# Performance work log

Hardware: AMD Instinct MI355X
Metric: run time of the kernel (lower is better)

Reference implementation:

```python
import jax, jax.numpy as jnp
import numpy as np

ALPHA = 0.2          # LeakyReLU slope
THRESH = 0.6         # adjacency connection threshold
NEG_INF = -9e15      # masked-softmax fill used by the original


def setup_inputs() -> dict:
    key = jax.random.key(0)
    ks = jax.random.split(key, 5)
    B, N, F = 32, 512, 128
    h = jax.random.normal(ks[0], (B, N, F), dtype=jnp.float32)
    # torch nn.Linear weights: y = x @ W.T
    W = jax.random.normal(ks[1], (F, F), dtype=jnp.float32) * 0.1
    a = jax.random.normal(ks[2], (2 * F, 1), dtype=jnp.float32) * 0.1
    A0 = jax.random.normal(ks[3], (4 * N, N), dtype=jnp.float32) * 0.05
    A2 = jax.random.normal(ks[4], (N, 4 * N), dtype=jnp.float32) * 0.05
    return {"h": h, "W": W, "a": a, "A0": A0, "A2": A2}


def reference(h, W, a, A0, A2):
    F = W.shape[0]
    # Wh = W(h)                                  [B, N, F]
    Wh = jnp.einsum("bnf,gf->bng", h, W)
    # attention logits e = leakyrelu(Wh a1 + (Wh a2)^T)   [B, N, N]
    Wh1 = Wh @ a[:F]                              # [B, N, 1]
    Wh2 = Wh @ a[F:]                              # [B, N, 1]
    e = jax.nn.leaky_relu(Wh1 + jnp.swapaxes(Wh2, 1, 2), ALPHA)
    # learned adjacency MLP over last (node) dim: Linear -> Sigmoid -> Linear
    adj = e + jnp.einsum("bnk,mk->bnm", jax.nn.sigmoid(jnp.einsum("bnm,km->bnk", e, A0)), A2)
    # threshold + mask + softmax
    adj = jnp.where(adj > THRESH, adj, 0.0)
    att = jnp.where(adj > 0, e, NEG_INF)
    att = jax.nn.softmax(att, axis=2)
    # dropout is identity in eval mode
    h_prime = jnp.einsum("bnm,bmf->bnf", att, Wh)
    return jax.nn.elu(h_prime)                    # concat=True branch
```

## Files before the change

kernel.cpp:

```cpp
#include <hip/hip_runtime.h>

#define BB 32
#define NN 512
#define FF 128
#define K4 2048
#define ALPHA 0.2f
#define THRESH 0.6f
#define NEGINF -9e15f

typedef unsigned short u16;
typedef unsigned int u32;
typedef _Float16 f16;
typedef __attribute__((ext_vector_type(8))) _Float16 half8;
typedef __attribute__((ext_vector_type(4))) float f32x4;

union U16F { u16 u; f16 h; };
__device__ __forceinline__ u16 hbits(f16 h) { U16F x; x.h = h; return x.u; }
__device__ __forceinline__ float htof(u16 u) { U16F x; x.u = u; return (float)x.h; }
__device__ __forceinline__ void split2(float v, u16& hi, u16& lo) {
    f16 h = (f16)v;
    f16 l = (f16)(v - (float)h);
    hi = hbits(h);
    lo = hbits(l);
}
__device__ __forceinline__ float lrelu(float x) { return x > 0.f ? x : ALPHA * x; }

__device__ __forceinline__ void gload16(const void* g, void* l) {
    __builtin_amdgcn_global_load_lds(
        (__attribute__((address_space(1))) const unsigned int*)(unsigned long long)g,
        (__attribute__((address_space(3))) unsigned int*)(unsigned int)(unsigned long long)l,
        16, 0, 0);
}

__global__ void k_u(const float* __restrict__ W, const float* __restrict__ a,
                    float* __restrict__ u12) {
    int f = threadIdx.x;
    float s1 = 0.f, s2 = 0.f;
    for (int g = 0; g < FF; ++g) {
        float w = W[g * FF + f];
        s1 += w * a[g];
        s2 += w * a[FF + g];
    }
    u12[f] = s1;
    u12[FF + f] = s2;
}

__global__ void k_wh12(const float* __restrict__ h, const float* __restrict__ u12,
                       float* __restrict__ Wh12) {
    int row = blockIdx.x;
    int f = threadIdx.x;
    float hv = h[(size_t)row * FF + f];
    float p1 = hv * u12[f], p2 = hv * u12[FF + f];
#pragma unroll
    for (int o = 1; o < 64; o <<= 1) {
        p1 += __shfl_xor(p1, o, 64);
        p2 += __shfl_xor(p2, o, 64);
    }
    __shared__ float s1[2], s2[2];
    int w = f >> 6;
    if ((f & 63) == 0) { s1[w] = p1; s2[w] = p2; }
    __syncthreads();
    if (f == 0) {
        Wh12[row] = s1[0] + s1[1];
        Wh12[BB * NN + row] = s2[0] + s2[1];
    }
}

__global__ __launch_bounds__(256) void k_whT(const float* __restrict__ W,
                                             const float* __restrict__ h,
                                             u16* __restrict__ Thi, u16* __restrict__ Tlo) {
    const int bm = blockIdx.y * 64, bn = blockIdx.x * 64;
    __shared__ float As[32][68];
    __shared__ float Bs[32][68];
    int tid = threadIdx.x;
    int tx = tid & 15, ty = tid >> 4;
    float acc[4][4] = {{0.f}};
    int r = tid >> 3, q = tid & 7;
    const float* Ap = W + (size_t)(bm + r) * FF + q * 4;
    const float* Bp = h + (size_t)(bn + r) * FF + q * 4;
    for (int k0 = 0; k0 < FF; k0 += 32) {
        float4 a0 = *(const float4*)(Ap + k0);
        float4 a1 = *(const float4*)(Ap + k0 + 32 * FF);
        float4 b0 = *(const float4*)(Bp + k0);
        float4 b1 = *(const float4*)(Bp + k0 + 32 * FF);
        __syncthreads();
        As[q * 4 + 0][r] = a0.x; As[q * 4 + 1][r] = a0.y;
        As[q * 4 + 2][r] = a0.z; As[q * 4 + 3][r] = a0.w;
        As[q * 4 + 0][r + 32] = a1.x; As[q * 4 + 1][r + 32] = a1.y;
        As[q * 4 + 2][r + 32] = a1.z; As[q * 4 + 3][r + 32] = a1.w;
        Bs[q * 4 + 0][r] = b0.x; Bs[q * 4 + 1][r] = b0.y;
        Bs[q * 4 + 2][r] = b0.z; Bs[q * 4 + 3][r] = b0.w;
        Bs[q * 4 + 0][r + 32] = b1.x; Bs[q * 4 + 1][r + 32] = b1.y;
        Bs[q * 4 + 2][r + 32] = b1.z; Bs[q * 4 + 3][r + 32] = b1.w;
        __syncthreads();
#pragma unroll
        for (int kk = 0; kk < 32; ++kk) {
            float av[4], bv[4];
            *(float4*)av = *(const float4*)&As[kk][ty * 4];
            *(float4*)bv = *(const float4*)&Bs[kk][tx * 4];
#pragma unroll
            for (int i = 0; i < 4; ++i)
#pragma unroll
                for (int j = 0; j < 4; ++j) acc[i][j] = fmaf(av[i], bv[j], acc[i][j]);
        }
    }
#pragma unroll
    for (int i = 0; i < 4; ++i) {
        int f = bm + ty * 4 + i;
#pragma unroll
        for (int j = 0; j < 4; ++j) {
            int mg = bn + tx * 4 + j;
            u16 hi, lo;
            split2(acc[i][j], hi, lo);
            size_t idx = ((size_t)(mg >> 9) * FF + f) * NN + (mg & 511);
            Thi[idx] = hi;
            Tlo[idx] = lo;
        }
    }
}

__global__ void k_split(const float* __restrict__ X, u16* __restrict__ Hi,
                        u16* __restrict__ Lo, int n4) {
    int i = blockIdx.x * 256 + threadIdx.x;
    if (i >= n4) return;
    float4 v = *(const float4*)(X + (size_t)i * 4);
    ushort4 hh, ll;
    split2(v.x, hh.x, ll.x);
    split2(v.y, hh.y, ll.y);
    split2(v.z, hh.z, ll.z);
    split2(v.w, hh.w, ll.w);
    *(ushort4*)(Hi + (size_t)i * 4) = hh;
    *(ushort4*)(Lo + (size_t)i * 4) = ll;
}

__global__ __launch_bounds__(512, 2) void k_g1(const float* __restrict__ Wh12, int c0,
                                               const u16* __restrict__ Bhi,
                                               const u16* __restrict__ Blo,
                                               u16* __restrict__ Shi, u16* __restrict__ Slo,
                                               int mblocks) {
    __shared__ __align__(16) u16 lds[2][4][8192];
    __shared__ float wh1s[256];
    __shared__ float wh2s[512];
    const int tid = threadIdx.x;
    const int l = tid & 63, w = tid >> 6;
    const int nwg = gridDim.x, q = nwg >> 3;
    const int wg = (blockIdx.x & 7) * q + (blockIdx.x >> 3);
    const int nb = wg / mblocks, mb = wg % mblocks;
    const int bm = mb * 256, bn = nb * 256;
    const int bglob = c0 + (bm >> 9);

    if (tid < 256) wh1s[tid] = Wh12[(size_t)c0 * NN + bm + tid];
    wh2s[tid] = Wh12[BB * NN + (size_t)bglob * NN + tid];
    if (tid + 512 < 512) {}
    __syncthreads();

    auto GEN_A = [&](int buf, int k0) {
#pragma unroll
        for (int cc = 0; cc < 2; ++cc) {
            const int c = tid + cc * 512;
            const int row = ((c >> 6) << 4) + (c & 15);
            const int kc = k0 + ((c >> 4) & 3) * 8;
            const float w1 = wh1s[row];
            u32 hh[4], llv[4];
#pragma unroll
            for (int jj = 0; jj < 4; ++jj) {
                float e0 = lrelu(w1 + wh2s[kc + 2 * jj]);
                float e1 = lrelu(w1 + wh2s[kc + 2 * jj + 1]);
                u16 h0, l0, h1, l1;
                split2(e0, h0, l0);
                split2(e1, h1, l1);
                hh[jj] = (u32)h0 | ((u32)h1 << 16);
                llv[jj] = (u32)l0 | ((u32)l1 << 16);
            }
            *(uint4*)&lds[buf][0][c * 8] = make_uint4(hh[0], hh[1], hh[2], hh[3]);
            *(uint4*)&lds[buf][1][c * 8] = make_uint4(llv[0], llv[1], llv[2], llv[3]);
        }
    };
    auto STAGE_B = [&](int buf, int k0) {
#pragma unroll
        for (int i = 0; i < 2; ++i) {
            const int g = w * 2 + i;
            const size_t ro = (size_t)(bn + g * 16 + (l & 15)) * NN + k0 + ((l >> 4) * 8);
            gload16(Bhi + ro, &lds[buf][2][g * 512]);
            gload16(Blo + ro, &lds[buf][3][g * 512]);
        }
    };

    f32x4 acc[8][4];
#pragma unroll
    for (int m = 0; m < 8; ++m)
#pragma unroll
        for (int n = 0; n < 4; ++n) acc[m][n] = (f32x4){0.f, 0.f, 0.f, 0.f};

    GEN_A(0, 0);
    STAGE_B(0, 0);
    for (int t = 0; t < 16; ++t) {
        const int cur = t & 1;
        if (t < 15) {
            GEN_A(cur ^ 1, (t + 1) * 32);
            STAGE_B(cur ^ 1, (t + 1) * 32);
            asm volatile("s_waitcnt vmcnt(4)" ::: "memory");
        } else {
            asm volatile("s_waitcnt vmcnt(0)" ::: "memory");
        }
        asm volatile("s_waitcnt lgkmcnt(0)" ::: "memory");
        __builtin_amdgcn_s_barrier();
        __builtin_amdgcn_sched_barrier(0);
        half8 bh[4], bl[4];
#pragma unroll
        for (int n = 0; n < 4; ++n) {
            const int gB = (w & 3) * 4 + n;
            bh[n] = *(const half8*)&lds[cur][2][(gB * 64 + l) * 8];
            bl[n] = *(const half8*)&lds[cur][3][(gB * 64 + l) * 8];
        }
        __builtin_amdgcn_s_setprio(1);
#pragma unroll
        for (int m = 0; m < 8; ++m) {
            const int gA = (w >> 2) * 8 + m;
            half8 ah = *(const half8*)&lds[cur][0][(gA * 64 + l) * 8];
            half8 al = *(const half8*)&lds[cur][1][(gA * 64 + l) * 8];
#pragma unroll
            for (int n = 0; n < 4; ++n) {
                acc[m][n] =
                    __builtin_amdgcn_mfma_f32_16x16x32_f16(ah, bh[n], acc[m][n], 0, 0, 0);
                acc[m][n] =
                    __builtin_amdgcn_mfma_f32_16x16x32_f16(al, bh[n], acc[m][n], 0, 0, 0);
                acc[m][n] =
                    __builtin_amdgcn_mfma_f32_16x16x32_f16(ah, bl[n], acc[m][n], 0, 0, 0);
            }
        }
        __builtin_amdgcn_s_setprio(0);
        __builtin_amdgcn_sched_barrier(0);
        __builtin_amdgcn_s_barrier();
    }

    const int lr = (l >> 4) * 4, lc = l & 15;
#pragma unroll
    for (int m = 0; m < 8; ++m) {
#pragma unroll
        for (int n = 0; n < 4; ++n) {
#pragma unroll
            for (int j = 0; j < 4; ++j) {
                const int row = bm + (w >> 2) * 128 + m * 16 + lr + j;
                const int col = bn + (w & 3) * 64 + n * 16 + lc;
                const float s = 1.f / (1.f + expf(-acc[m][n][j]));
                u16 hi, lo;
                split2(s, hi, lo);
                const size_t idx = (size_t)row * K4 + col;
                Shi[idx] = hi;
                Slo[idx] = lo;
            }
        }
    }
}

__global__ __launch_bounds__(512, 2) void k_g2(const u16* __restrict__ Ahi,
                                               const u16* __restrict__ Alo,
                                               const u16* __restrict__ Bhi,
                                               const u16* __restrict__ Blo,
                                               const float* __restrict__ Wh12, int c0,
                                               u32* __restrict__ ADJ, int mblocks) {
    __shared__ __align__(16) u16 ldsA[2][2][4096];
    __shared__ __align__(16) u16 ldsB[2][2][8192];
    const int tid = threadIdx.x;
    const int l = tid & 63, w = tid >> 6;
    const int nwg = gridDim.x, q = nwg >> 3;
    const int wg = (blockIdx.x & 7) * q + (blockIdx.x >> 3);
    const int nb = wg / mblocks, mb = wg % mblocks;
    const int bm = mb * 128, bn = nb * 256;

    auto STAGE = [&](int buf, int k0) {
        const size_t ra = (size_t)(bm + w * 16 + (l & 15)) * K4 + k0 + ((l >> 4) * 8);
        gload16(Ahi + ra, &ldsA[buf][0][w * 512]);
        gload16(Alo + ra, &ldsA[buf][1][w * 512]);
#pragma unroll
        for (int i = 0; i < 2; ++i) {
            const int g = w * 2 + i;
            const size_t rb = (size_t)(bn + g * 16 + (l & 15)) * K4 + k0 + ((l >> 4) * 8);
            gload16(Bhi + rb, &ldsB[buf][0][g * 512]);
            gload16(Blo + rb, &ldsB[buf][1][g * 512]);
        }
    };

    f32x4 acc[4][4];
#pragma unroll
    for (int m = 0; m < 4; ++m)
#pragma unroll
        for (int n = 0; n < 4; ++n) acc[m][n] = (f32x4){0.f, 0.f, 0.f, 0.f};

    STAGE(0, 0);
    for (int t = 0; t < 64; ++t) {
        const int cur = t & 1;
        if (t < 63) {
            STAGE(cur ^ 1, (t + 1) * 32);
            asm volatile("s_waitcnt vmcnt(6)" ::: "memory");
        } else {
            asm volatile("s_waitcnt vmcnt(0)" ::: "memory");
        }
        __builtin_amdgcn_s_barrier();
        __builtin_amdgcn_sched_barrier(0);
        half8 bh[4], bl[4];
#pragma unroll
        for (int n = 0; n < 4; ++n) {
            const int gB = (w & 3) * 4 + n;
            bh[n] = *(const half8*)&ldsB[cur][0][(gB * 64 + l) * 8];
            bl[n] = *(const half8*)&ldsB[cur][1][(gB * 64 + l) * 8];
        }
        __builtin_amdgcn_s_setprio(1);
#pragma unroll
        for (int m = 0; m < 4; ++m) {
            const int gA = (w >> 2) * 4 + m;
            half8 ah = *(const half8*)&ldsA[cur][0][(gA * 64 + l) * 8];
            half8 al = *(const half8*)&ldsA[cur][1][(gA * 64 + l) * 8];
#pragma unroll
            for (int n = 0; n < 4; ++n) {
                acc[m][n] =
                    __builtin_amdgcn_mfma_f32_16x16x32_f16(ah, bh[n], acc[m][n], 0, 0, 0);
                acc[m][n] =
                    __builtin_amdgcn_mfma_f32_16x16x32_f16(al, bh[n], acc[m][n], 0, 0, 0);
                acc[m][n] =
                    __builtin_amdgcn_mfma_f32_16x16x32_f16(ah, bl[n], acc[m][n], 0, 0, 0);
            }
        }
        __builtin_amdgcn_s_setprio(0);
        __builtin_amdgcn_sched_barrier(0);
        __builtin_amdgcn_s_barrier();
    }

    const int bglob = c0 + (bm >> 9);
    const float* wh2p = Wh12 + BB * NN + (size_t)bglob * NN;
    const int lr = (l >> 4) * 4, lc = l & 15;
#pragma unroll
    for (int m = 0; m < 4; ++m) {
#pragma unroll
        for (int n = 0; n < 4; ++n) {
#pragma unroll
            for (int j = 0; j < 4; ++j) {
                const int row = bm + (w >> 2) * 64 + m * 16 + lr + j;
                const int col = bn + (w & 3) * 64 + n * 16 + lc;
                const float e = lrelu(Wh12[(size_t)c0 * NN + row] + wh2p[col]);
                u32 pk = 0xFFFFFFFFu;
                if (e + acc[m][n][j] > THRESH) {
                    u16 hi, lo;
                    split2(e, hi, lo);
                    pk = (u32)hi | ((u32)lo << 16);
                }
                ADJ[(size_t)row * NN + col] = pk;
            }
        }
    }
}

__global__ __launch_bounds__(256) void k_softmax2(const u32* __restrict__ ADJ,
                                                  u16* __restrict__ Hi, u16* __restrict__ Lo) {
    const size_t row = blockIdx.x;
    const u32* p = ADJ + row * NN;
    const int t = threadIdx.x;
    u32 w0 = p[t], w1 = p[t + 256];
    float v0 = (w0 == 0xFFFFFFFFu) ? NEGINF : htof((u16)(w0 & 0xFFFF)) + htof((u16)(w0 >> 16));
    float v1 = (w1 == 0xFFFFFFFFu) ? NEGINF : htof((u16)(w1 & 0xFFFF)) + htof((u16)(w1 >> 16));
    float m = fmaxf(v0, v1);
#pragma unroll
    for (int o = 1; o < 64; o <<= 1) m = fmaxf(m, __shfl_xor(m, o, 64));
    __shared__ float red[4], red2[4];
    int w = t >> 6;
    if ((t & 63) == 0) red[w] = m;
    __syncthreads();
    m = fmaxf(fmaxf(red[0], red[1]), fmaxf(red[2], red[3]));
    float e0 = __expf(v0 - m), e1 = __expf(v1 - m);
    float s = e0 + e1;
#pragma unroll
    for (int o = 1; o < 64; o <<= 1) s += __shfl_xor(s, o, 64);
    if ((t & 63) == 0) red2[w] = s;
    __syncthreads();
    s = red2[0] + red2[1] + red2[2] + red2[3];
    float inv = 1.f / s;
    float a0 = e0 * inv, a1 = e1 * inv;
    u16 h0, l0, h1, l1;
    split2(a0, h0, l0);
    split2(a1, h1, l1);
    Hi[row * NN + t] = h0;
    Hi[row * NN + t + 256] = h1;
    Lo[row * NN + t] = l0;
    Lo[row * NN + t + 256] = l1;
}

__global__ __launch_bounds__(256) void k_pv(const u16* __restrict__ Ahi,
                                            const u16* __restrict__ Alo,
                                            const u16* __restrict__ Bhi,
                                            const u16* __restrict__ Blo,
                                            float* __restrict__ OUT) {
    __shared__ __align__(16) u16 lds[2][4][4096];
    const int tid = threadIdx.x;
    const int l = tid & 63, w = tid >> 6;
    const int wr = w >> 1, wc = w & 1;
    const int bz = blockIdx.z;
    const int bm = blockIdx.y * 128, bn = 0;

    const u16* A0p = Ahi + (size_t)bz * NN * NN;
    const u16* A1p = Alo + (size_t)bz * NN * NN;
    const u16* B0p = Bhi + (size_t)bz * FF * NN;
    const u16* B1p = Blo + (size_t)bz * FF * NN;

    const int g0 = w, g1 = w + 4;
    const size_t offA0 = (size_t)(bm + g0 * 16 + (l & 15)) * NN + (l >> 4) * 8;
    const size_t offA1 = (size_t)(bm + g1 * 16 + (l & 15)) * NN + (l >> 4) * 8;
    const size_t offB0 = (size_t)(bn + g0 * 16 + (l & 15)) * NN + (l >> 4) * 8;
    const size_t offB1 = (size_t)(bn + g1 * 16 + (l & 15)) * NN + (l >> 4) * 8;

    auto STAGE = [&](int buf, int kk) {
        gload16(A0p + offA0 + kk, &lds[buf][0][g0 * 512]);
        gload16(A0p + offA1 + kk, &lds[buf][0][g1 * 512]);
        gload16(A1p + offA0 + kk, &lds[buf][1][g0 * 512]);
        gload16(A1p + offA1 + kk, &lds[buf][1][g1 * 512]);
        gload16(B0p + offB0 + kk, &lds[buf][2][g0 * 512]);
        gload16(B0p + offB1 + kk, &lds[buf][2][g1 * 512]);
        gload16(B1p + offB0 + kk, &lds[buf][3][g0 * 512]);
        gload16(B1p + offB1 + kk, &lds[buf][3][g1 * 512]);
    };

    f32x4 acc[4][4];
#pragma unroll
    for (int m = 0; m < 4; ++m)
#pragma unroll
        for (int n = 0; n < 4; ++n) acc[m][n] = (f32x4){0.f, 0.f, 0.f, 0.f};

    STAGE(0, 0);
    for (int t = 0; t < 16; ++t) {
        const int cur = t & 1;
        if (t + 1 < 16) {
            STAGE(cur ^ 1, (t + 1) * 32);
            asm volatile("s_waitcnt vmcnt(8)" ::: "memory");
        } else {
            asm volatile("s_waitcnt vmcnt(0)" ::: "memory");
        }
        __builtin_amdgcn_s_barrier();
        __builtin_amdgcn_sched_barrier(0);
        half8 ah[4], al[4], bh[4], bl[4];
#pragma unroll
        for (int m = 0; m < 4; ++m) {
            ah[m] = *(const half8*)&lds[cur][0][((wr * 4 + m) * 64 + l) * 8];
            al[m] = *(const half8*)&lds[cur][1][((wr * 4 + m) * 64 + l) * 8];
        }
#pragma unroll
        for (int n = 0; n < 4; ++n) {
            bh[n] = *(const half8*)&lds[cur][2][((wc * 4 + n) * 64 + l) * 8];
            bl[n] = *(const half8*)&lds[cur][3][((wc * 4 + n) * 64 + l) * 8];
        }
#pragma unroll
        for (int m = 0; m < 4; ++m)
#pragma unroll
            for (int n = 0; n < 4; ++n) {
                acc[m][n] =
                    __builtin_amdgcn_mfma_f32_16x16x32_f16(ah[m], bh[n], acc[m][n], 0, 0, 0);
                acc[m][n] =
                    __builtin_amdgcn_mfma_f32_16x16x32_f16(al[m], bh[n], acc[m][n], 0, 0, 0);
                acc[m][n] =
                    __builtin_amdgcn_mfma_f32_16x16x32_f16(ah[m], bl[n], acc[m][n], 0, 0, 0);
            }
        __builtin_amdgcn_s_barrier();
    }

    const int lr = (l >> 4) * 4, lc = l & 15;
#pragma unroll
    for (int m = 0; m < 4; ++m) {
#pragma unroll
        for (int n = 0; n < 4; ++n) {
#pragma unroll
            for (int j = 0; j < 4; ++j) {
                const int row = bm + wr * 64 + m * 16 + lr + j;
                const int col = bn + wc * 64 + n * 16 + lc;
                const float v = acc[m][n][j];
                OUT[(size_t)bz * NN * FF + (size_t)row * FF + col] =
                    v > 0.f ? v : __expf(v) - 1.f;
            }
        }
    }
}

extern "C" void kernel_launch(void* const* d_in, const int* in_sizes, int n_in,
                              void* d_out, int out_size, void* d_ws, size_t ws_size,
                              hipStream_t stream) {
    const float* h = (const float*)d_in[0];
    const float* W = (const float*)d_in[1];
    const float* a = (const float*)d_in[2];
    const float* A0 = (const float*)d_in[3];
    const float* A2 = (const float*)d_in[4];
    float* out = (float*)d_out;

    char* ws = (char*)d_ws;
    size_t ofs = 0;
    auto alloc = [&](size_t bytes) -> void* {
        void* p = ws + ofs;
        ofs = (ofs + bytes + 255) & ~(size_t)255;
        return p;
    };
    float* u12 = (float*)alloc(2 * FF * sizeof(float));
    float* Wh12 = (float*)alloc(2 * (size_t)BB * NN * sizeof(float));
    u16* WhThi = (u16*)alloc((size_t)BB * FF * NN * 2);
    u16* WhTlo = (u16*)alloc((size_t)BB * FF * NN * 2);
    u16* A0hi = (u16*)alloc((size_t)K4 * NN * 2);
    u16* A0lo = (u16*)alloc((size_t)K4 * NN * 2);
    u16* A2hi = (u16*)alloc((size_t)NN * K4 * 2);
    u16* A2lo = (u16*)alloc((size_t)NN * K4 * 2);

    const size_t per_b =
        (size_t)NN * K4 * 2 * 2 + (size_t)NN * NN * 4 + (size_t)NN * NN * 2 * 2;
    int cb = BB;
    while (cb > 1 && ofs + (size_t)cb * per_b + 8192 > ws_size) cb >>= 1;
    u16* Shi = (u16*)alloc((size_t)cb * NN * K4 * 2);
    u16* Slo = (u16*)alloc((size_t)cb * NN * K4 * 2);
    u32* ADJ = (u32*)alloc((size_t)cb * NN * NN * 4);
    u16* AttHi = (u16*)alloc((size_t)cb * NN * NN * 2);
    u16* AttLo = (u16*)alloc((size_t)cb * NN * NN * 2);

    k_u<<<1, 128, 0, stream>>>(W, a, u12);
    k_wh12<<<BB * NN, 128, 0, stream>>>(h, u12, Wh12);
    k_whT<<<dim3((BB * NN) / 64, FF / 64), 256, 0, stream>>>(W, h, WhThi, WhTlo);
    k_split<<<(K4 * NN / 4 + 255) / 256, 256, 0, stream>>>(A0, A0hi, A0lo, K4 * NN / 4);
    k_split<<<(NN * K4 / 4 + 255) / 256, 256, 0, stream>>>(A2, A2hi, A2lo, NN * K4 / 4);

    for (int c0 = 0; c0 < BB; c0 += cb) {
        const int c = (BB - c0) < cb ? (BB - c0) : cb;
        const int mb1 = c * 2;
        const int mb2 = c * 4;
        k_g1<<<mb1 * (K4 / 256), 512, 0, stream>>>(Wh12, c0, A0hi, A0lo, Shi, Slo, mb1);
        k_g2<<<mb2 * (NN / 256), 512, 0, stream>>>(Shi, Slo, A2hi, A2lo, Wh12, c0, ADJ, mb2);
        k_softmax2<<<c * NN, 256, 0, stream>>>(ADJ, AttHi, AttLo);
        k_pv<<<dim3(1, NN / 128, c), 256, 0, stream>>>(
            AttHi, AttLo, WhThi + (size_t)c0 * FF * NN, WhTlo + (size_t)c0 * FF * NN,
            out + (size_t)c0 * NN * FF);
    }
}
```

Baseline: 292.2 us.

## Ping-pong wave halves in k_g1 so A-tile generation overlaps MFMA

In k_g1, the two halves of the workgroup (p=0/1) now take turns: one half runs the MFMA block while the other generates its own rows of the next A tile (leaky-ReLU logits split into fp16 hi/lo), with a barrier between phases. Each half generates exactly the A rows it consumes, and wh2 values are read once per lane as float4 vectors. The MFMA issue order is reordered so that independent accumulators sit between dependent MFMAs, in k_g1, k_g2 and the final GEMM. Smaller changes: lrelu becomes fmaxf and the sigmoid uses __expf. The aim is to hide VALU generation cost behind matrix work, at the cost of an extra barrier per k-step and full vmcnt waits.

```diff
diff --git a/kernel.cpp b/kernel.cpp
--- a/kernel.cpp
+++ b/kernel.cpp
@@ -23,7 +23,7 @@
     hi = hbits(h);
     lo = hbits(l);
 }
-__device__ __forceinline__ float lrelu(float x) { return x > 0.f ? x : ALPHA * x; }
+__device__ __forceinline__ float lrelu(float x) { return fmaxf(x, ALPHA * x); }
 
 __device__ __forceinline__ void gload16(const void* g, void* l) {
     __builtin_amdgcn_global_load_lds(
@@ -143,6 +143,7 @@
     __shared__ float wh2s[512];
     const int tid = threadIdx.x;
     const int l = tid & 63, w = tid >> 6;
+    const int p = w >> 2, wq = w & 3;
     const int nwg = gridDim.x, q = nwg >> 3;
     const int wg = (blockIdx.x & 7) * q + (blockIdx.x >> 3);
     const int nb = wg / mblocks, mb = wg % mblocks;
@@ -151,99 +152,103 @@
 
     if (tid < 256) wh1s[tid] = Wh12[(size_t)c0 * NN + bm + tid];
     wh2s[tid] = Wh12[BB * NN + (size_t)bglob * NN + tid];
-    if (tid + 512 < 512) {}
     __syncthreads();
 
-    auto GEN_A = [&](int buf, int k0) {
-#pragma unroll
-        for (int cc = 0; cc < 2; ++cc) {
-            const int c = tid + cc * 512;
-            const int row = ((c >> 6) << 4) + (c & 15);
-            const int kc = k0 + ((c >> 4) & 3) * 8;
-            const float w1 = wh1s[row];
+    f32x4 acc[8][4];
+#pragma unroll
+    for (int m = 0; m < 8; ++m)
+#pragma unroll
+        for (int n = 0; n < 4; ++n) acc[m][n] = (f32x4){0.f, 0.f, 0.f, 0.f};
+
+    auto STAGE_MINE = [&](int buf, int k0) {
+#pragma unroll
+        for (int i = 0; i < 2; ++i) {
+            const int g = p * 8 + wq * 2 + i;
+            const size_t ro = (size_t)(bn + g * 16 + (l & 15)) * NN + k0 + ((l >> 4) * 8);
+            gload16(Bhi + ro, &lds[buf][2][g * 512]);
+            gload16(Blo + ro, &lds[buf][3][g * 512]);
+        }
+    };
+    auto GEN_MINE = [&](int buf, int k0) {
+        const int kc = k0 + (l >> 4) * 8;
+        float w2v[8];
+        *(float4*)&w2v[0] = *(const float4*)&wh2s[kc];
+        *(float4*)&w2v[4] = *(const float4*)&wh2s[kc + 4];
+#pragma unroll
+        for (int i = 0; i < 2; ++i) {
+            const int g = p * 8 + wq * 2 + i;
+            const float w1 = wh1s[g * 16 + (l & 15)];
             u32 hh[4], llv[4];
 #pragma unroll
             for (int jj = 0; jj < 4; ++jj) {
-                float e0 = lrelu(w1 + wh2s[kc + 2 * jj]);
-                float e1 = lrelu(w1 + wh2s[kc + 2 * jj + 1]);
+                float e0 = lrelu(w1 + w2v[2 * jj]);
+                float e1 = lrelu(w1 + w2v[2 * jj + 1]);
                 u16 h0, l0, h1, l1;
                 split2(e0, h0, l0);
                 split2(e1, h1, l1);
                 hh[jj] = (u32)h0 | ((u32)h1 << 16);
                 llv[jj] = (u32)l0 | ((u32)l1 << 16);
             }
-            *(uint4*)&lds[buf][0][c * 8] = make_uint4(hh[0], hh[1], hh[2], hh[3]);
-            *(uint4*)&lds[buf][1][c * 8] = make_uint4(llv[0], llv[1], llv[2], llv[3]);
+            *(uint4*)&lds[buf][0][(g * 64 + l) * 8] = make_uint4(hh[0], hh[1], hh[2], hh[3]);
+            *(uint4*)&lds[buf][1][(g * 64 + l) * 8] = make_uint4(llv[0], llv[1], llv[2], llv[3]);
         }
     };
-    auto STAGE_B = [&](int buf, int k0) {
-#pragma unroll
-        for (int i = 0; i < 2; ++i) {
-            const int g = w * 2 + i;
-            const size_t ro = (size_t)(bn + g * 16 + (l & 15)) * NN + k0 + ((l >> 4) * 8);
-            gload16(Bhi + ro, &lds[buf][2][g * 512]);
-            gload16(Blo + ro, &lds[buf][3][g * 512]);
-        }
+    auto DO_MFMA = [&](int cur) {
+        half8 bh[4], bl[4];
+#pragma unroll
+        for (int n = 0; n < 4; ++n) {
+            const int gB = wq * 4 + n;
+            bh[n] = *(const half8*)&lds[cur][2][(gB * 64 + l) * 8];
+            bl[n] = *(const half8*)&lds[cur][3][(gB * 64 + l) * 8];
+        }
+        __builtin_amdgcn_s_setprio(1);
+#pragma unroll
+        for (int m = 0; m < 8; ++m) {
+            const int gA = p * 8 + m;
+            half8 ah = *(const half8*)&lds[cur][0][(gA * 64 + l) * 8];
+            half8 al = *(const half8*)&lds[cur][1][(gA * 64 + l) * 8];
+#pragma unroll
+            for (int n = 0; n < 4; ++n)
+                acc[m][n] = __builtin_amdgcn_mfma_f32_16x16x32_f16(ah, bh[n], acc[m][n], 0, 0, 0);
+#pragma unroll
+            for (int n = 0; n < 4; ++n)
+                acc[m][n] = __builtin_amdgcn_mfma_f32_16x16x32_f16(al, bh[n], acc[m][n], 0, 0, 0);
+#pragma unroll
+            for (int n = 0; n < 4; ++n)
+                acc[m][n] = __builtin_amdgcn_mfma_f32_16x16x32_f16(ah, bl[n], acc[m][n], 0, 0, 0);
+        }
+        __builtin_amdgcn_s_setprio(0);
     };
 
-    f32x4 acc[8][4];
-#pragma unroll
-    for (int m = 0; m < 8; ++m)
-#pragma unroll
-        for (int n = 0; n < 4; ++n) acc[m][n] = (f32x4){0.f, 0.f, 0.f, 0.f};
-
-    GEN_A(0, 0);
-    STAGE_B(0, 0);
+    STAGE_MINE(0, 0);
+    GEN_MINE(0, 0);
+    asm volatile("s_waitcnt vmcnt(0) lgkmcnt(0)" ::: "memory");
+    __syncthreads();
+
     for (int t = 0; t < 16; ++t) {
-        const int cur = t & 1;
-        if (t < 15) {
-            GEN_A(cur ^ 1, (t + 1) * 32);
-            STAGE_B(cur ^ 1, (t + 1) * 32);
-            asm volatile("s_waitcnt vmcnt(4)" ::: "memory");
-        } else {
-            asm volatile("s_waitcnt vmcnt(0)" ::: "memory");
-        }
+        const int cur = t & 1, k1 = (t + 1) * 32;
+        const bool more = (t < 15);
+        if (more) STAGE_MINE(cur ^ 1, k1);
+        if (p == 0) DO_MFMA(cur);
+        else if (more) GEN_MINE(cur ^ 1, k1);
         asm volatile("s_waitcnt lgkmcnt(0)" ::: "memory");
         __builtin_amdgcn_s_barrier();
-        __builtin_amdgcn_sched_barrier(0);
-        half8 bh[4], bl[4];
+        if (p == 1) DO_MFMA(cur);
+        else if (more) GEN_MINE(cur ^ 1, k1);
+        asm volatile("s_waitcnt vmcnt(0) lgkmcnt(0)" ::: "memory");
+        __builtin_amdgcn_s_barrier();
+    }
+
+    const int lr = (l >> 4) * 4, lc = l & 15;
+#pragma unroll
+    for (int m = 0; m < 8; ++m) {
 #pragma unroll
         for (int n = 0; n < 4; ++n) {
-            const int gB = (w & 3) * 4 + n;
-            bh[n] = *(const half8*)&lds[cur][2][(gB * 64 + l) * 8];
-            bl[n] = *(const half8*)&lds[cur][3][(gB * 64 + l) * 8];
-        }
-        __builtin_amdgcn_s_setprio(1);
-#pragma unroll
-        for (int m = 0; m < 8; ++m) {
-            const int gA = (w >> 2) * 8 + m;
-            half8 ah = *(const half8*)&lds[cur][0][(gA * 64 + l) * 8];
-            half8 al = *(const half8*)&lds[cur][1][(gA * 64 + l) * 8];
-#pragma unroll
-            for (int n = 0; n < 4; ++n) {
-                acc[m][n] =
-                    __builtin_amdgcn_mfma_f32_16x16x32_f16(ah, bh[n], acc[m][n], 0, 0, 0);
-                acc[m][n] =
-                    __builtin_amdgcn_mfma_f32_16x16x32_f16(al, bh[n], acc[m][n], 0, 0, 0);
-                acc[m][n] =
-                    __builtin_amdgcn_mfma_f32_16x16x32_f16(ah, bl[n], acc[m][n], 0, 0, 0);
-            }
-        }
-        __builtin_amdgcn_s_setprio(0);
-        __builtin_amdgcn_sched_barrier(0);
-        __builtin_amdgcn_s_barrier();
-    }
-
-    const int lr = (l >> 4) * 4, lc = l & 15;
-#pragma unroll
-    for (int m = 0; m < 8; ++m) {
-#pragma unroll
-        for (int n = 0; n < 4; ++n) {
 #pragma unroll
             for (int j = 0; j < 4; ++j) {
-                const int row = bm + (w >> 2) * 128 + m * 16 + lr + j;
-                const int col = bn + (w & 3) * 64 + n * 16 + lc;
-                const float s = 1.f / (1.f + expf(-acc[m][n][j]));
+                const int row = bm + p * 128 + m * 16 + lr + j;
+                const int col = bn + wq * 64 + n * 16 + lc;
+                const float s = 1.f / (1.f + __expf(-acc[m][n][j]));
                 u16 hi, lo;
                 split2(s, hi, lo);
                 const size_t idx = (size_t)row * K4 + col;
@@ -313,14 +318,14 @@
             half8 ah = *(const half8*)&ldsA[cur][0][(gA * 64 + l) * 8];
             half8 al = *(const half8*)&ldsA[cur][1][(gA * 64 + l) * 8];
 #pragma unroll
-            for (int n = 0; n < 4; ++n) {
-                acc[m][n] =
-                    __builtin_amdgcn_mfma_f32_16x16x32_f16(ah, bh[n], acc[m][n], 0, 0, 0);
-                acc[m][n] =
-                    __builtin_amdgcn_mfma_f32_16x16x32_f16(al, bh[n], acc[m][n], 0, 0, 0);
-                acc[m][n] =
-                    __builtin_amdgcn_mfma_f32_16x16x32_f16(ah, bl[n], acc[m][n], 0, 0, 0);
-            }
+            for (int n = 0; n < 4; ++n)
+                acc[m][n] = __builtin_amdgcn_mfma_f32_16x16x32_f16(ah, bh[n], acc[m][n], 0, 0, 0);
+#pragma unroll
+            for (int n = 0; n < 4; ++n)
+                acc[m][n] = __builtin_amdgcn_mfma_f32_16x16x32_f16(al, bh[n], acc[m][n], 0, 0, 0);
+#pragma unroll
+            for (int n = 0; n < 4; ++n)
+                acc[m][n] = __builtin_amdgcn_mfma_f32_16x16x32_f16(ah, bl[n], acc[m][n], 0, 0, 0);
         }
         __builtin_amdgcn_s_setprio(0);
         __builtin_amdgcn_sched_barrier(0);
@@ -448,16 +453,19 @@
             bl[n] = *(const half8*)&lds[cur][3][((wc * 4 + n) * 64 + l) * 8];
         }
 #pragma unroll
-        for (int m = 0; m < 4; ++m)
+        for (int m = 0; m < 4; ++m) {
+#pragma unroll
+            for (int n = 0; n < 4; ++n)
+                acc[m][n] = __builtin_amdgcn_mfma_f32_16x16x32_f16(ah[m], bh[n], acc[m][n], 0, 0, 0);
+        }
+#pragma unroll
+        for (int m = 0; m < 4; ++m) {
 #pragma unroll
             for (int n = 0; n < 4; ++n) {
-                acc[m][n] =
-                    __builtin_amdgcn_mfma_f32_16x16x32_f16(ah[m], bh[n], acc[m][n], 0, 0, 0);
-                acc[m][n] =
-                    __builtin_amdgcn_mfma_f32_16x16x32_f16(al[m], bh[n], acc[m][n], 0, 0, 0);
-                acc[m][n] =
-                    __builtin_amdgcn_mfma_f32_16x16x32_f16(ah[m], bl[n], acc[m][n], 0, 0, 0);
+                acc[m][n] = __builtin_amdgcn_mfma_f32_16x16x32_f16(al[m], bh[n], acc[m][n], 0, 0, 0);
+                acc[m][n] = __builtin_amdgcn_mfma_f32_16x16x32_f16(ah[m], bl[n], acc[m][n], 0, 0, 0);
             }
+        }
         __builtin_amdgcn_s_barrier();
     }
 
```

Result: faster. 282.3 us (-3.4%).
